# Optimization experiments

Measured on AMD Instinct MI355X. Metric: run time of the kernel, lower is better.

Reference implementation:

```python
import jax, jax.numpy as jnp
import numpy as np

DIM = 192
NUM_HEADS = 6
KERNELS = [3, 5, 7]
DILATIONS = [1, 2, 3]
NBRANCH = 3
HEADS_B = NUM_HEADS // NBRANCH      # heads per branch = 2
HEAD_DIM = DIM // NUM_HEADS         # 32


def _axis_idx(L, K, d):
    """NATTEN-style neighborhood indices along one axis with dilation.
    Returns (nbr[L,K] absolute neighbor positions, bias[L,K] rpb indices in [0, 2K-2]).
    """
    i = np.arange(L)
    g = i % d                                 # dilation group
    ii = i // d                               # index within subgrid
    Lg = (L - g + d - 1) // d                 # subgrid length of each group
    start = np.clip(ii - K // 2, 0, Lg - K)   # clamp window inside bounds
    ki = np.arange(K)
    nbr = g[:, None] + (start[:, None] + ki[None, :]) * d        # [L,K]
    bias = start[:, None] + ki[None, :] - ii[:, None] + (K - 1)  # [L,K]
    return nbr, bias


def _branch(xb, K, d, rpb):
    # xb: [B,H,W, 3*heads*head_dim] laid out as (3, heads, head_dim)
    B, H, W, _ = xb.shape
    qkv = xb.reshape(B, H, W, 3, HEADS_B, HEAD_DIM).transpose(3, 0, 4, 1, 2, 5)
    q, k, v = qkv[0], qkv[1], qkv[2]          # [B,h,H,W,hd]
    q = q * (HEAD_DIM ** -0.5)
    nh, bh = _axis_idx(H, K, d)
    nw, bw = _axis_idx(W, K, d)
    # gather K x K neighborhoods: [B,h,H,W,K,K,hd]
    k_nb = k[:, :, nh[:, None, :, None], nw[None, :, None, :]]
    attn = jnp.einsum('bhijd,bhijkld->bhijkl', q, k_nb)
    attn = attn + rpb[:, bh[:, None, :, None], bw[None, :, None, :]][None]
    attn = jax.nn.softmax(attn.reshape(B, HEADS_B, H, W, K * K), axis=-1)
    attn = attn.reshape(B, HEADS_B, H, W, K, K)
    v_nb = v[:, :, nh[:, None, :, None], nw[None, :, None, :]]
    y = jnp.einsum('bhijkl,bhijkld->bhijd', attn, v_nb)
    return y.transpose(0, 2, 3, 1, 4).reshape(B, H, W, HEADS_B * HEAD_DIM)


def setup_inputs() -> dict:
    key = jax.random.key(0)
    ks = jax.random.split(key, 8)
    B, H, W = 8, 64, 64
    return {
        'x': jax.random.normal(ks[0], (B, DIM, H, W), jnp.float32),
        'qkv_w': jax.random.normal(ks[1], (3 * DIM, DIM), jnp.float32) * 0.02,
        'qkv_b': jnp.zeros((3 * DIM,), jnp.float32),
        'proj_w': jax.random.normal(ks[2], (DIM, DIM), jnp.float32) * 0.02,
        'proj_b': jnp.zeros((DIM,), jnp.float32),
        'rpb0': jax.random.normal(ks[3], (HEADS_B, 5, 5), jnp.float32) * 0.02,
        'rpb1': jax.random.normal(ks[4], (HEADS_B, 9, 9), jnp.float32) * 0.02,
        'rpb2': jax.random.normal(ks[5], (HEADS_B, 13, 13), jnp.float32) * 0.02,
    }


def reference(x, qkv_w, qkv_b, proj_w, proj_b, rpb0, rpb1, rpb2):
    # x: [B,C,H,W] -> BHWC
    xp = x.transpose(0, 2, 3, 1)
    qkv = xp @ qkv_w.T + qkv_b                 # [B,H,W,3*dim]
    branches = jnp.split(qkv, NBRANCH, axis=-1)  # equal channels (dim divisible by k)
    rpbs = [rpb0, rpb1, rpb2]
    ys = [_branch(branches[i], KERNELS[i], DILATIONS[i], rpbs[i]) for i in range(NBRANCH)]
    out = jnp.concatenate(ys, axis=-1) @ proj_w.T + proj_b
    return out.transpose(0, 3, 1, 2)
```

## Files before the change

### kernel.cpp

```cpp
#include <hip/hip_runtime.h>
#include <stdint.h>

typedef __attribute__((ext_vector_type(4))) float f32x4;
typedef _Float16 half8 __attribute__((ext_vector_type(8)));
typedef _Float16 half2v __attribute__((ext_vector_type(2)));

#define LDK 200
#define QSCALE 0.17677669529663689f

__device__ __forceinline__ float dot2f(unsigned int k2, unsigned int q2, float c) {
#if __has_builtin(__builtin_amdgcn_fdot2)
  return __builtin_amdgcn_fdot2(__builtin_bit_cast(half2v, k2),
                                __builtin_bit_cast(half2v, q2), c, false);
#else
  half2v a = __builtin_bit_cast(half2v, k2), b = __builtin_bit_cast(half2v, q2);
  return c + (float)a.x * (float)b.x + (float)a.y * (float)b.y;
#endif
}

__global__ __launch_bounds__(256) void prep_w(
    const float* __restrict__ qw, const float* __restrict__ qb,
    _Float16* __restrict__ qwh, float* __restrict__ qbs) {
  int i = blockIdx.x * 256 + threadIdx.x;
  if (i < 27648) {
    float4 v = ((const float4*)qw)[i];
    int n = (i * 4) / 192;
    float sc = ((n % 192) < 64) ? QSCALE : 1.0f;
    _Float16* d = qwh + i * 4;
    d[0] = (_Float16)(v.x * sc); d[1] = (_Float16)(v.y * sc);
    d[2] = (_Float16)(v.z * sc); d[3] = (_Float16)(v.w * sc);
  } else if (i < 27648 + 576) {
    int n = i - 27648;
    qbs[n] = qb[n] * (((n % 192) < 64) ? QSCALE : 1.0f);
  }
}

__global__ __launch_bounds__(256) void qkv_gemm(
    const float* __restrict__ x, const _Float16* __restrict__ wh,
    const float* __restrict__ qbs, _Float16* __restrict__ qkv) {
  __shared__ _Float16 Al[64 * LDK];
  const int t = threadIdx.x;
  const int tm = blockIdx.x;
  const int bb = (tm * 64) >> 12, hw0 = (tm * 64) & 4095;
  const float* xb = x + (size_t)bb * 192 * 4096 + hw0;

  #pragma unroll
  for (int j = 0; j < 12; ++j) {
    int idx = j * 256 + t;
    int m4 = (idx & 15) * 4, c = idx >> 4;
    float4 v = *(const float4*)(xb + (size_t)c * 4096 + m4);
    Al[(m4 + 0) * LDK + c] = (_Float16)v.x;
    Al[(m4 + 1) * LDK + c] = (_Float16)v.y;
    Al[(m4 + 2) * LDK + c] = (_Float16)v.z;
    Al[(m4 + 3) * LDK + c] = (_Float16)v.w;
  }
  __syncthreads();

  const int lane = t & 63, wid = t >> 6;
  const int wm = (wid >> 1) * 32, wn = (wid & 1) * 32;
  const int lr = lane & 15, kb = (lane >> 4) * 8;
  const int r0 = (lane >> 4) * 4;
  _Float16* opb = qkv + (size_t)(tm * 64) * 576;

  for (int n0 = 0; n0 < 576; n0 += 64) {
    f32x4 acc[2][2];
    #pragma unroll
    for (int i = 0; i < 2; ++i)
      #pragma unroll
      for (int j = 0; j < 2; ++j)
        #pragma unroll
        for (int r = 0; r < 4; ++r) acc[i][j][r] = 0.0f;

    #pragma unroll
    for (int kk = 0; kk < 192; kk += 32) {
      half8 a0 = *(const half8*)&Al[(wm + lr) * LDK + kk + kb];
      half8 a1 = *(const half8*)&Al[(wm + 16 + lr) * LDK + kk + kb];
      half8 b0 = *(const half8*)(wh + (size_t)(n0 + wn + lr) * 192 + kk + kb);
      half8 b1 = *(const half8*)(wh + (size_t)(n0 + wn + 16 + lr) * 192 + kk + kb);
      acc[0][0] = __builtin_amdgcn_mfma_f32_16x16x32_f16(a0, b0, acc[0][0], 0, 0, 0);
      acc[0][1] = __builtin_amdgcn_mfma_f32_16x16x32_f16(a0, b1, acc[0][1], 0, 0, 0);
      acc[1][0] = __builtin_amdgcn_mfma_f32_16x16x32_f16(a1, b0, acc[1][0], 0, 0, 0);
      acc[1][1] = __builtin_amdgcn_mfma_f32_16x16x32_f16(a1, b1, acc[1][1], 0, 0, 0);
    }

    #pragma unroll
    for (int i = 0; i < 2; ++i)
      #pragma unroll
      for (int j = 0; j < 2; ++j) {
        int gn = n0 + wn + j * 16 + lr;
        float bs = qbs[gn];
        #pragma unroll
        for (int r = 0; r < 4; ++r) {
          int row = wm + i * 16 + r0 + r;
          opb[row * 576 + gn] = (_Float16)(acc[i][j][r] + bs);
        }
      }
  }
}

template <int K, int DIL>
__device__ __forceinline__ void natten_branch(
    const _Float16* __restrict__ qkv, const float* __restrict__ rpb,
    _Float16* __restrict__ yo, const int branch, const int r,
    unsigned short* __restrict__ smem) {
  constexpr int RW = 2 * K - 1;
  constexpr int H8 = K + 7;
  constexpr int NH = H8 * H8;
  constexpr int NL = (K * K + 3) / 4;
  constexpr int LSTR = 40;

  _Float16* Kl = (_Float16*)smem;
  _Float16* Vl = Kl + NH * LSTR;
  _Float16* Ql = Vl + NH * LSTR;
  float* rs = (float*)(Ql + 64 * LSTR);

  const int t = threadIdx.x;
  const int bh = r & 15;
  const int head = bh & 1, bb = bh >> 1;
  const int rr = r >> 4;
  int gh, gw, ti, tj, Lgh, Lgw;
  if (DIL == 1) {
    gh = 0; gw = 0; ti = (rr >> 3) * 8; tj = (rr & 7) * 8; Lgh = 64; Lgw = 64;
  } else if (DIL == 2) {
    int cls = rr >> 4, tile = rr & 15;
    gh = cls >> 1; gw = cls & 1; ti = (tile >> 2) * 8; tj = (tile & 3) * 8;
    Lgh = 32; Lgw = 32;
  } else {
    int cls = rr / 9, tile = rr % 9;
    gh = cls / 3; gw = cls % 3; ti = (tile / 3) * 8; tj = (tile % 3) * 8;
    Lgh = (64 - gh + 2) / 3; Lgw = (64 - gw + 2) / 3;
  }
  const int hoh = max(0, min(ti - K / 2, Lgh - K));
  const int how = max(0, min(tj - K / 2, Lgw - K));

  for (int i = t; i < RW * RW; i += 256) rs[i] = rpb[head * RW * RW + i];

  const _Float16* kvb = qkv + (size_t)bb * 4096 * 576 + branch * 192 + 64 + head * 32;
  for (int L = t; L < NH * 8; L += 256) {
    int px = L >> 3, part = L & 7;
    int hr = px / H8, hc = px % H8;
    int cr = min(hoh + hr, Lgh - 1), cc = min(how + hc, Lgw - 1);
    int ph = gh + cr * DIL, pw2 = gw + cc * DIL;
    const _Float16* src = kvb + (size_t)(ph * 64 + pw2) * 576 + (part & 3) * 8 + ((part & 4) ? 64 : 0);
    _Float16* dst = ((part & 4) ? Vl : Kl) + px * LSTR + (part & 3) * 8;
    *(uint4*)dst = *(const uint4*)src;
  }
  {
    int qi = t >> 2, part = t & 3;
    int ci0 = min(ti + (qi >> 3), Lgh - 1), cj0 = min(tj + (qi & 7), Lgw - 1);
    int ph = gh + ci0 * DIL, pw2 = gw + cj0 * DIL;
    const _Float16* src = qkv + (size_t)((size_t)bb * 4096 + ph * 64 + pw2) * 576
                          + branch * 192 + head * 32 + part * 8;
    *(uint4*)(Ql + qi * LSTR + part * 8) = *(const uint4*)src;
  }
  __syncthreads();

  const int qi = t >> 2, sl = t & 3;
  const int ci = ti + (qi >> 3), cj = tj + (qi & 7);
  const bool valid = (ci < Lgh) && (cj < Lgw);

  int s0h = ci - K / 2; if (s0h < 0) s0h = 0; if (s0h > Lgh - K) s0h = Lgh - K;
  int s0w = cj - K / 2; if (s0w < 0) s0w = 0; if (s0w > Lgw - K) s0w = Lgw - K;
  const int rbase = s0h - hoh, cbase = s0w - how;
  const int bhb = s0h - ci + K - 1, bwb = s0w - cj + K - 1;

  unsigned int qh[16];
  #pragma unroll
  for (int u = 0; u < 4; ++u) {
    uint4 v = *(const uint4*)(Ql + qi * LSTR + u * 8);
    qh[u * 4 + 0] = v.x; qh[u * 4 + 1] = v.y; qh[u * 4 + 2] = v.z; qh[u * 4 + 3] = v.w;
  }

  float s[NL];
  float mx = -1e30f;
  #pragma unroll
  for (int j = 0; j < NL; ++j) {
    int n = sl + 4 * j;
    if (n < K * K) {
      int kh = n / K, kw = n % K;
      int lidx = (rbase + kh) * H8 + (cbase + kw);
      const _Float16* kp = Kl + lidx * LSTR;
      float sc = rs[(bhb + kh) * RW + (bwb + kw)];
      #pragma unroll
      for (int u = 0; u < 4; ++u) {
        uint4 kv = *(const uint4*)(kp + u * 8);
        sc = dot2f(kv.x, qh[4 * u + 0], sc);
        sc = dot2f(kv.y, qh[4 * u + 1], sc);
        sc = dot2f(kv.z, qh[4 * u + 2], sc);
        sc = dot2f(kv.w, qh[4 * u + 3], sc);
      }
      s[j] = sc;
      mx = fmaxf(mx, sc);
    } else {
      s[j] = -1e30f;
    }
  }
  mx = fmaxf(mx, __shfl_xor(mx, 1, 64));
  mx = fmaxf(mx, __shfl_xor(mx, 2, 64));

  float pw[NL];
  float l = 0.0f;
  #pragma unroll
  for (int j = 0; j < NL; ++j) { pw[j] = __expf(s[j] - mx); l += pw[j]; }
  l += __shfl_xor(l, 1, 64);
  l += __shfl_xor(l, 2, 64);

  half2v acch[16];
  #pragma unroll
  for (int i = 0; i < 16; ++i) acch[i] = (half2v)(_Float16)0.0f;
  #pragma unroll
  for (int j = 0; j < NL; ++j) {
    int n = sl + 4 * j;
    if (n < K * K) {
      int kh = n / K, kw = n % K;
      int lidx = (rbase + kh) * H8 + (cbase + kw);
      const _Float16* vp = Vl + lidx * LSTR;
      _Float16 ph = (_Float16)pw[j];
      half2v pp = {ph, ph};
      #pragma unroll
      for (int u = 0; u < 4; ++u) {
        uint4 vv = *(const uint4*)(vp + u * 8);
        acch[4 * u + 0] += pp * __builtin_bit_cast(half2v, vv.x);
        acch[4 * u + 1] += pp * __builtin_bit_cast(half2v, vv.y);
        acch[4 * u + 2] += pp * __builtin_bit_cast(half2v, vv.z);
        acch[4 * u + 3] += pp * __builtin_bit_cast(half2v, vv.w);
      }
    }
  }
  #pragma unroll
  for (int st = 1; st <= 2; st <<= 1) {
    #pragma unroll
    for (int i = 0; i < 16; ++i) {
      unsigned int o = __shfl_xor(__builtin_bit_cast(unsigned int, acch[i]), st, 64);
      acch[i] += __builtin_bit_cast(half2v, o);
    }
  }

  if (valid) {
    float inv = 1.0f / l;
    _Float16 ih = (_Float16)inv;
    half2v iv = {ih, ih};
    unsigned int a[16];
    #pragma unroll
    for (int i = 0; i < 16; ++i) a[i] = __builtin_bit_cast(unsigned int, acch[i]);
    uint4 pk;
    unsigned int r0, r1, r2, r3;
    r0 = (sl < 2) ? ((sl == 0) ? a[0] : a[4]) : ((sl == 2) ? a[8] : a[12]);
    r1 = (sl < 2) ? ((sl == 0) ? a[1] : a[5]) : ((sl == 2) ? a[9] : a[13]);
    r2 = (sl < 2) ? ((sl == 0) ? a[2] : a[6]) : ((sl == 2) ? a[10] : a[14]);
    r3 = (sl < 2) ? ((sl == 0) ? a[3] : a[7]) : ((sl == 2) ? a[11] : a[15]);
    pk.x = __builtin_bit_cast(unsigned int, __builtin_bit_cast(half2v, r0) * iv);
    pk.y = __builtin_bit_cast(unsigned int, __builtin_bit_cast(half2v, r1) * iv);
    pk.z = __builtin_bit_cast(unsigned int, __builtin_bit_cast(half2v, r2) * iv);
    pk.w = __builtin_bit_cast(unsigned int, __builtin_bit_cast(half2v, r3) * iv);
    const int p = bb * 4096 + (gh + ci * DIL) * 64 + (gw + cj * DIL);
    *(uint4*)(yo + (size_t)p * 192 + branch * 64 + head * 32 + sl * 8) = pk;
  }
}

__global__ __launch_bounds__(256) void natten_all(
    const _Float16* __restrict__ qkv,
    const float* __restrict__ rpb0, const float* __restrict__ rpb1,
    const float* __restrict__ rpb2, _Float16* __restrict__ yo) {
  __shared__ __align__(16) unsigned short smem[18624];
  const int gid = blockIdx.x;
  if (gid < 1296)       natten_branch<7, 3>(qkv, rpb2, yo, 2, gid, smem);
  else if (gid < 2320)  natten_branch<5, 2>(qkv, rpb1, yo, 1, gid - 1296, smem);
  else                  natten_branch<3, 1>(qkv, rpb0, yo, 0, gid - 2320, smem);
}

__global__ __launch_bounds__(256) void proj_gemm(
    const _Float16* __restrict__ y, const float* __restrict__ w,
    const float* __restrict__ bias, float* __restrict__ out) {
  __shared__ _Float16 Al[64 * LDK];
  __shared__ _Float16 Bl[64 * LDK];
  const int t = threadIdx.x;
  const int tp = blockIdx.x;

  const _Float16* ybp = y + (size_t)(tp * 64) * 192;
  #pragma unroll
  for (int j = 0; j < 6; ++j) {
    int idx = j * 256 + t;
    int m = idx / 24, k8 = (idx % 24) * 8;
    *(uint4*)&Bl[m * LDK + k8] = *(const uint4*)(ybp + m * 192 + k8);
  }

  const int lane = t & 63, wid = t >> 6;
  const int wm = (wid >> 1) * 32, wn = (wid & 1) * 32;
  const int lr = lane & 15, kb = (lane >> 4) * 8;
  const int r0 = (lane >> 4) * 4;
  const int gp = tp * 64;
  const int bb = gp >> 12, hw0 = gp & 4095;
  float* op = out + (size_t)bb * 192 * 4096 + hw0;

  for (int c0 = 0; c0 < 192; c0 += 64) {
    if (c0) __syncthreads();
    #pragma unroll
    for (int j = 0; j < 12; ++j) {
      int idx = j * 256 + t;
      int n = idx / 48, k = (idx % 48) * 4;
      const float4 wv = *(const float4*)(w + (size_t)(c0 + n) * 192 + k);
      Al[n * LDK + k + 0] = (_Float16)wv.x;
      Al[n * LDK + k + 1] = (_Float16)wv.y;
      Al[n * LDK + k + 2] = (_Float16)wv.z;
      Al[n * LDK + k + 3] = (_Float16)wv.w;
    }
    __syncthreads();

    f32x4 acc[2][2];
    #pragma unroll
    for (int i = 0; i < 2; ++i)
      #pragma unroll
      for (int j = 0; j < 2; ++j)
        #pragma unroll
        for (int r = 0; r < 4; ++r) acc[i][j][r] = 0.0f;

    #pragma unroll
    for (int kk = 0; kk < 192; kk += 32) {
      half8 a0 = *(const half8*)&Al[(wm + lr) * LDK + kk + kb];
      half8 a1 = *(const half8*)&Al[(wm + 16 + lr) * LDK + kk + kb];
      half8 b0 = *(const half8*)&Bl[(wn + lr) * LDK + kk + kb];
      half8 b1 = *(const half8*)&Bl[(wn + 16 + lr) * LDK + kk + kb];
      acc[0][0] = __builtin_amdgcn_mfma_f32_16x16x32_f16(a0, b0, acc[0][0], 0, 0, 0);
      acc[0][1] = __builtin_amdgcn_mfma_f32_16x16x32_f16(a0, b1, acc[0][1], 0, 0, 0);
      acc[1][0] = __builtin_amdgcn_mfma_f32_16x16x32_f16(a1, b0, acc[1][0], 0, 0, 0);
      acc[1][1] = __builtin_amdgcn_mfma_f32_16x16x32_f16(a1, b1, acc[1][1], 0, 0, 0);
    }

    #pragma unroll
    for (int i = 0; i < 2; ++i)
      #pragma unroll
      for (int j = 0; j < 2; ++j) {
        int m = wn + j * 16 + lr;
        #pragma unroll
        for (int r = 0; r < 4; ++r) {
          int c = c0 + wm + i * 16 + r0 + r;
          op[(size_t)c * 4096 + m] = acc[i][j][r] + bias[c];
        }
      }
  }
}

extern "C" void kernel_launch(void* const* d_in, const int* in_sizes, int n_in,
                              void* d_out, int out_size, void* d_ws, size_t ws_size,
                              hipStream_t stream) {
  const float* x      = (const float*)d_in[0];
  const float* qkv_w  = (const float*)d_in[1];
  const float* qkv_b  = (const float*)d_in[2];
  const float* proj_w = (const float*)d_in[3];
  const float* proj_b = (const float*)d_in[4];
  const float* rpb0   = (const float*)d_in[5];
  const float* rpb1   = (const float*)d_in[6];
  const float* rpb2   = (const float*)d_in[7];

  _Float16* qkv = (_Float16*)d_ws;
  _Float16* yb  = (_Float16*)d_ws + (size_t)32768 * 576;
  _Float16* qwh = (_Float16*)d_out;
  float*    qbs = (float*)((char*)d_out + 221184);
  float* out = (float*)d_out;

  prep_w<<<dim3(111), 256, 0, stream>>>(qkv_w, qkv_b, qwh, qbs);
  qkv_gemm<<<dim3(512), 256, 0, stream>>>(x, qwh, qbs, qkv);
  natten_all<<<dim3(3344), 256, 0, stream>>>(qkv, rpb0, rpb1, rpb2, yb);
  proj_gemm<<<dim3(512), 256, 0, stream>>>(yb, proj_w, proj_b, out);
}
```

Before: 158.1 us.

## Split QKV and proj GEMMs across output-column grid, pre-convert proj weights to fp16

Both GEMM kernels gain a second grid dimension of 3, so each block computes one third of the output columns instead of looping over all of them. This raises block count from 512 to 1536 for better occupancy and latency hiding. The proj weights are now converted to fp16 once in prep_w and read directly from global memory as MFMA A operands, which drops a per-block LDS staging pass and two barriers. The trade-off is that qkv_gemm reloads and transposes the x tile three times and proj_gemm reloads the y tile three times. Scratch buffers move from d_out into the workspace.

```diff
diff --git a/kernel.cpp b/kernel.cpp
--- a/kernel.cpp
+++ b/kernel.cpp
@@ -20,7 +20,8 @@
 
 __global__ __launch_bounds__(256) void prep_w(
     const float* __restrict__ qw, const float* __restrict__ qb,
-    _Float16* __restrict__ qwh, float* __restrict__ qbs) {
+    const float* __restrict__ pw,
+    _Float16* __restrict__ qwh, float* __restrict__ qbs, _Float16* __restrict__ pwh) {
   int i = blockIdx.x * 256 + threadIdx.x;
   if (i < 27648) {
     float4 v = ((const float4*)qw)[i];
@@ -29,8 +30,14 @@
     _Float16* d = qwh + i * 4;
     d[0] = (_Float16)(v.x * sc); d[1] = (_Float16)(v.y * sc);
     d[2] = (_Float16)(v.z * sc); d[3] = (_Float16)(v.w * sc);
-  } else if (i < 27648 + 576) {
-    int n = i - 27648;
+  } else if (i < 36864) {
+    int k = i - 27648;
+    float4 v = ((const float4*)pw)[k];
+    _Float16* d = pwh + k * 4;
+    d[0] = (_Float16)v.x; d[1] = (_Float16)v.y;
+    d[2] = (_Float16)v.z; d[3] = (_Float16)v.w;
+  } else if (i < 36864 + 576) {
+    int n = i - 36864;
     qbs[n] = qb[n] * (((n % 192) < 64) ? QSCALE : 1.0f);
   }
 }
@@ -41,6 +48,7 @@
   __shared__ _Float16 Al[64 * LDK];
   const int t = threadIdx.x;
   const int tm = blockIdx.x;
+  const int ng = blockIdx.y;
   const int bb = (tm * 64) >> 12, hw0 = (tm * 64) & 4095;
   const float* xb = x + (size_t)bb * 192 * 4096 + hw0;
 
@@ -62,7 +70,7 @@
   const int r0 = (lane >> 4) * 4;
   _Float16* opb = qkv + (size_t)(tm * 64) * 576;
 
-  for (int n0 = 0; n0 < 576; n0 += 64) {
+  for (int n0 = ng * 192; n0 < ng * 192 + 192; n0 += 64) {
     f32x4 acc[2][2];
     #pragma unroll
     for (int i = 0; i < 2; ++i)
@@ -270,12 +278,12 @@
 }
 
 __global__ __launch_bounds__(256) void proj_gemm(
-    const _Float16* __restrict__ y, const float* __restrict__ w,
+    const _Float16* __restrict__ y, const _Float16* __restrict__ wh,
     const float* __restrict__ bias, float* __restrict__ out) {
-  __shared__ _Float16 Al[64 * LDK];
   __shared__ _Float16 Bl[64 * LDK];
   const int t = threadIdx.x;
   const int tp = blockIdx.x;
+  const int c0 = blockIdx.y * 64;
 
   const _Float16* ybp = y + (size_t)(tp * 64) * 192;
   #pragma unroll
@@ -284,6 +292,7 @@
     int m = idx / 24, k8 = (idx % 24) * 8;
     *(uint4*)&Bl[m * LDK + k8] = *(const uint4*)(ybp + m * 192 + k8);
   }
+  __syncthreads();
 
   const int lane = t & 63, wid = t >> 6;
   const int wm = (wid >> 1) * 32, wn = (wid & 1) * 32;
@@ -293,52 +302,37 @@
   const int bb = gp >> 12, hw0 = gp & 4095;
   float* op = out + (size_t)bb * 192 * 4096 + hw0;
 
-  for (int c0 = 0; c0 < 192; c0 += 64) {
-    if (c0) __syncthreads();
-    #pragma unroll
-    for (int j = 0; j < 12; ++j) {
-      int idx = j * 256 + t;
-      int n = idx / 48, k = (idx % 48) * 4;
-      const float4 wv = *(const float4*)(w + (size_t)(c0 + n) * 192 + k);
-      Al[n * LDK + k + 0] = (_Float16)wv.x;
-      Al[n * LDK + k + 1] = (_Float16)wv.y;
-      Al[n * LDK + k + 2] = (_Float16)wv.z;
-      Al[n * LDK + k + 3] = (_Float16)wv.w;
-    }
-    __syncthreads();
-
-    f32x4 acc[2][2];
-    #pragma unroll
-    for (int i = 0; i < 2; ++i)
-      #pragma unroll
-      for (int j = 0; j < 2; ++j)
-        #pragma unroll
-        for (int r = 0; r < 4; ++r) acc[i][j][r] = 0.0f;
-
-    #pragma unroll
-    for (int kk = 0; kk < 192; kk += 32) {
-      half8 a0 = *(const half8*)&Al[(wm + lr) * LDK + kk + kb];
-      half8 a1 = *(const half8*)&Al[(wm + 16 + lr) * LDK + kk + kb];
-      half8 b0 = *(const half8*)&Bl[(wn + lr) * LDK + kk + kb];
-      half8 b1 = *(const half8*)&Bl[(wn + 16 + lr) * LDK + kk + kb];
-      acc[0][0] = __builtin_amdgcn_mfma_f32_16x16x32_f16(a0, b0, acc[0][0], 0, 0, 0);
-      acc[0][1] = __builtin_amdgcn_mfma_f32_16x16x32_f16(a0, b1, acc[0][1], 0, 0, 0);
-      acc[1][0] = __builtin_amdgcn_mfma_f32_16x16x32_f16(a1, b0, acc[1][0], 0, 0, 0);
-      acc[1][1] = __builtin_amdgcn_mfma_f32_16x16x32_f16(a1, b1, acc[1][1], 0, 0, 0);
-    }
-
-    #pragma unroll
-    for (int i = 0; i < 2; ++i)
-      #pragma unroll
-      for (int j = 0; j < 2; ++j) {
-        int m = wn + j * 16 + lr;
-        #pragma unroll
-        for (int r = 0; r < 4; ++r) {
-          int c = c0 + wm + i * 16 + r0 + r;
-          op[(size_t)c * 4096 + m] = acc[i][j][r] + bias[c];
-        }
+  f32x4 acc[2][2];
+  #pragma unroll
+  for (int i = 0; i < 2; ++i)
+    #pragma unroll
+    for (int j = 0; j < 2; ++j)
+      #pragma unroll
+      for (int r = 0; r < 4; ++r) acc[i][j][r] = 0.0f;
+
+  #pragma unroll
+  for (int kk = 0; kk < 192; kk += 32) {
+    half8 a0 = *(const half8*)(wh + (size_t)(c0 + wm + lr) * 192 + kk + kb);
+    half8 a1 = *(const half8*)(wh + (size_t)(c0 + wm + 16 + lr) * 192 + kk + kb);
+    half8 b0 = *(const half8*)&Bl[(wn + lr) * LDK + kk + kb];
+    half8 b1 = *(const half8*)&Bl[(wn + 16 + lr) * LDK + kk + kb];
+    acc[0][0] = __builtin_amdgcn_mfma_f32_16x16x32_f16(a0, b0, acc[0][0], 0, 0, 0);
+    acc[0][1] = __builtin_amdgcn_mfma_f32_16x16x32_f16(a0, b1, acc[0][1], 0, 0, 0);
+    acc[1][0] = __builtin_amdgcn_mfma_f32_16x16x32_f16(a1, b0, acc[1][0], 0, 0, 0);
+    acc[1][1] = __builtin_amdgcn_mfma_f32_16x16x32_f16(a1, b1, acc[1][1], 0, 0, 0);
+  }
+
+  #pragma unroll
+  for (int i = 0; i < 2; ++i)
+    #pragma unroll
+    for (int j = 0; j < 2; ++j) {
+      int m = wn + j * 16 + lr;
+      #pragma unroll
+      for (int r = 0; r < 4; ++r) {
+        int c = c0 + wm + i * 16 + r0 + r;
+        op[(size_t)c * 4096 + m] = acc[i][j][r] + bias[c];
       }
-  }
+    }
 }
 
 extern "C" void kernel_launch(void* const* d_in, const int* in_sizes, int n_in,
@@ -354,13 +348,14 @@
   const float* rpb2   = (const float*)d_in[7];
 
   _Float16* qkv = (_Float16*)d_ws;
-  _Float16* yb  = (_Float16*)d_ws + (size_t)32768 * 576;
-  _Float16* qwh = (_Float16*)d_out;
-  float*    qbs = (float*)((char*)d_out + 221184);
+  _Float16* yb  = qkv + (size_t)32768 * 576;
+  _Float16* qwh = yb + (size_t)32768 * 192;
+  float*    qbs = (float*)(qwh + 110592);
+  _Float16* pwh = (_Float16*)(qbs + 576);
   float* out = (float*)d_out;
 
-  prep_w<<<dim3(111), 256, 0, stream>>>(qkv_w, qkv_b, qwh, qbs);
-  qkv_gemm<<<dim3(512), 256, 0, stream>>>(x, qwh, qbs, qkv);
+  prep_w<<<dim3(147), 256, 0, stream>>>(qkv_w, qkv_b, proj_w, qwh, qbs, pwh);
+  qkv_gemm<<<dim3(512, 3), 256, 0, stream>>>(x, qwh, qbs, qkv);
   natten_all<<<dim3(3344), 256, 0, stream>>>(qkv, rpb0, rpb1, rpb2, yb);
-  proj_gemm<<<dim3(512), 256, 0, stream>>>(yb, proj_w, proj_b, out);
-}
+  proj_gemm<<<dim3(512, 3), 256, 0, stream>>>(yb, pwh, proj_b, out);
+}
```

Result: no change. 161.0 us (+1.9%).
